# Kernel tuning notes

Hardware: AMD Instinct MI355X
Metric: run time of the kernel (lower is better)

The kernel has to match this reference:

```python
import jax, jax.numpy as jnp
import numpy as np
import math

IN_C, OUT_C, NUM_PARAM, STRIDE = 128, 256, 9, 1
BN_EPS = 1e-5


def _make_p_n(num_param):
    base_int = round(math.sqrt(num_param))
    row_number = num_param // base_int
    mod_number = num_param % base_int
    gx, gy = np.meshgrid(np.arange(row_number), np.arange(base_int), indexing='ij')
    px, py = gx.flatten(), gy.flatten()
    if mod_number > 0:
        mx, my = np.meshgrid(np.arange(row_number, row_number + 1), np.arange(mod_number), indexing='ij')
        px = np.concatenate([px, mx.flatten()])
        py = np.concatenate([py, my.flatten()])
    return np.concatenate([px, py]).astype(np.float32)  # (2N,)


def setup_inputs() -> dict:
    key = jax.random.key(0)
    ks = jax.random.split(key, 8)
    x = jax.random.normal(ks[0], (8, IN_C, 80, 80), dtype=jnp.float32)
    # offset-predicting conv (torch inits this to 0; use small random weights to exercise gathers)
    w_pconv = jax.random.normal(ks[1], (2 * NUM_PARAM, IN_C, 3, 3), dtype=jnp.float32) * 0.01
    b_pconv = jax.random.normal(ks[2], (2 * NUM_PARAM,), dtype=jnp.float32) * 0.1
    # final Conv: kernel (num_param, 1), stride (num_param, 1), pad 0, no bias
    w_conv = jax.random.normal(ks[3], (OUT_C, IN_C, NUM_PARAM, 1), dtype=jnp.float32) * (1.0 / math.sqrt(IN_C * NUM_PARAM))
    bn_gamma = jnp.ones((OUT_C,), jnp.float32) + 0.1 * jax.random.normal(ks[4], (OUT_C,), jnp.float32)
    bn_beta = 0.1 * jax.random.normal(ks[5], (OUT_C,), jnp.float32)
    bn_mean = 0.1 * jax.random.normal(ks[6], (OUT_C,), jnp.float32)
    bn_var = jnp.abs(jax.random.normal(ks[7], (OUT_C,), jnp.float32)) + 0.5
    p_n = jnp.asarray(_make_p_n(NUM_PARAM))
    return {"x": x, "w_pconv": w_pconv, "b_pconv": b_pconv, "w_conv": w_conv,
            "bn_gamma": bn_gamma, "bn_beta": bn_beta, "bn_mean": bn_mean,
            "bn_var": bn_var, "p_n": p_n}


def _conv2d(x, w, strides, padding):
    return jax.lax.conv_general_dilated(x, w, window_strides=strides, padding=padding,
                                        dimension_numbers=('NCHW', 'OIHW', 'NCHW'))


def reference(x, w_pconv, b_pconv, w_conv, bn_gamma, bn_beta, bn_mean, bn_var, p_n):
    b, c, H, W = x.shape
    # per-pixel offsets: [b, 2N, h, w]
    offset = _conv2d(x, w_pconv, (STRIDE, STRIDE), 'SAME') + b_pconv[None, :, None, None]
    N = offset.shape[1] // 2
    h, w = offset.shape[2], offset.shape[3]

    # sampling locations p = p_0 + p_n + offset
    px0 = jnp.broadcast_to((jnp.arange(h, dtype=x.dtype) * STRIDE)[None, None, :, None], (1, N, h, w))
    py0 = jnp.broadcast_to((jnp.arange(w, dtype=x.dtype) * STRIDE)[None, None, None, :], (1, N, h, w))
    p0 = jnp.concatenate([px0, py0], axis=1)  # [1, 2N, h, w]
    p = (p0 + p_n[None, :, None, None] + offset).transpose(0, 2, 3, 1)  # [b, h, w, 2N]

    def clamp2(t):
        return jnp.concatenate([jnp.clip(t[..., :N], 0, H - 1), jnp.clip(t[..., N:], 0, W - 1)], axis=-1)

    q_lt = clamp2(jnp.floor(p)).astype(jnp.int32)
    q_rb = clamp2(jnp.floor(p) + 1).astype(jnp.int32)
    q_lb = jnp.concatenate([q_lt[..., :N], q_rb[..., N:]], axis=-1)
    q_rt = jnp.concatenate([q_rb[..., :N], q_lt[..., N:]], axis=-1)
    pc = clamp2(p)

    # bilinear weights [b, h, w, N]
    def g(q, sx, sy):
        qf = q.astype(pc.dtype)
        return (1 + sx * (qf[..., :N] - pc[..., :N])) * (1 + sy * (qf[..., N:] - pc[..., N:]))

    g_lt, g_rb = g(q_lt, 1.0, 1.0), g(q_rb, -1.0, -1.0)
    g_lb, g_rt = g(q_lb, 1.0, -1.0), g(q_rt, -1.0, 1.0)

    x_flat = x.reshape(b, c, H * W)

    def gather(q):
        idx = (q[..., :N] * W + q[..., N:]).reshape(b, -1)  # [b, h*w*N]
        out = jax.vmap(lambda xf, i: xf[:, i])(x_flat, idx)  # [b, c, h*w*N]
        return out.reshape(b, c, h, w, N)

    x_off = (g_lt[:, None] * gather(q_lt) + g_rb[:, None] * gather(q_rb)
             + g_lb[:, None] * gather(q_lb) + g_rt[:, None] * gather(q_rt))

    # b c h w n -> b c (h n) w
    x_off = x_off.transpose(0, 1, 2, 4, 3).reshape(b, c, h * N, w)

    y = _conv2d(x_off, w_conv, (N, 1), 'VALID')  # [b, out_c, h, w]
    inv = jax.lax.rsqrt(bn_var + BN_EPS)
    y = (y - bn_mean[None, :, None, None]) * (bn_gamma * inv)[None, :, None, None] + bn_beta[None, :, None, None]
    return y * jax.nn.sigmoid(y)  # SiLU
```

## Files before the change

kernel.cpp:

```cpp
#include <hip/hip_runtime.h>
#include <hip/hip_bf16.h>


typedef __attribute__((ext_vector_type(8))) short bf16x8;
typedef __attribute__((ext_vector_type(4))) float f32x4;
typedef __attribute__((ext_vector_type(2))) float f32x2;
typedef __attribute__((ext_vector_type(4))) unsigned int u32x4;

#define NHW 6400
#define NPIX 80

__device__ __forceinline__ unsigned short f2bf(float f){
  __hip_bfloat16 h = __float2bfloat16(f);
  unsigned short u; __builtin_memcpy(&u, &h, 2); return u;
}
__device__ __forceinline__ f32x2 bfp2f(unsigned int u){
  union { unsigned int i; float f; } a, b;
  a.i = u << 16; b.i = u & 0xffff0000u;
  f32x2 r; r.x = a.f; r.y = b.f; return r;
}
__device__ __forceinline__ unsigned pk_bf16(float a, float b){
  unsigned r;
  asm("v_cvt_pk_bf16_f32 %0, %1, %2" : "=v"(r) : "v"(a), "v"(b));
  return r;
}
__device__ __forceinline__ void splitbf(float v, unsigned short& hi, unsigned short& lo){
  hi = f2bf(v);
  union { unsigned int i; float f; } h; h.i = (unsigned)hi << 16;
  lo = f2bf(v - h.f);
}
__device__ __forceinline__ float f16u2f(unsigned int u){
  unsigned short s = (unsigned short)u; _Float16 h;
  __builtin_memcpy(&h, &s, 2); return (float)h;
}
__device__ __forceinline__ unsigned short f2f16u(float f){
  _Float16 h = (_Float16)f; unsigned short s;
  __builtin_memcpy(&s, &h, 2); return s;
}
__device__ __forceinline__ float fast_silu(float v){
  float e, r;
  asm("v_exp_f32 %0, %1" : "=v"(e) : "v"(v * -1.44269504088896f));
  asm("v_rcp_f32 %0, %1" : "=v"(r) : "v"(1.0f + e));
  return v * r;
}

__global__ __launch_bounds__(256) void k_pre(const float* __restrict__ x,
                                             const float* __restrict__ w_conv,
                                             const float* __restrict__ w_pconv,
                                             const float* __restrict__ gamma,
                                             const float* __restrict__ beta,
                                             const float* __restrict__ mean,
                                             const float* __restrict__ var,
                                             unsigned short* __restrict__ xt,
                                             unsigned short* __restrict__ xtl,
                                             uint4* __restrict__ wf,
                                             uint4* __restrict__ wpfH,
                                             uint4* __restrict__ wpfL,
                                             float* __restrict__ shift){
  __shared__ unsigned short tileH[64 * 132];
  __shared__ unsigned short tileL[64 * 132];
  int blk = blockIdx.x; int t = threadIdx.x;
  if (blk < 800){
    int b = blk / 100; int pixbase = (blk % 100) * 64;
    int lane = t & 63; int cg = t >> 6;
    for (int ci = 0; ci < 32; ++ci){
      int c = cg * 32 + ci;
      float v = x[(b * 128 + c) * NHW + pixbase + lane];
      unsigned short hi, lo; splitbf(v, hi, lo);
      tileH[lane * 132 + c] = hi;
      tileL[lane * 132 + c] = lo;
    }
    __syncthreads();
    for (int i = 0; i < 8; ++i){
      int slot = t + i * 256; int m = slot >> 5; int c = (slot & 31) * 4;
      uint2 vH = *reinterpret_cast<const uint2*>(&tileH[m * 132 + c]);
      uint2 vL = *reinterpret_cast<const uint2*>(&tileL[m * 132 + c]);
      *reinterpret_cast<uint2*>(xt  + (b * NHW + pixbase + m) * 128 + c) = vH;
      *reinterpret_cast<uint2*>(xtl + (b * NHW + pixbase + m) * 128 + c) = vL;
    }
    return;
  }
  int pblk = blk - 800;
  if (pblk < 144){
    int id = pblk * 256 + t;
    int lane = id & 63, ofrag = (id >> 6) & 15, kc = (id >> 10) & 3, n = id >> 12;
    int o = ofrag * 16 + (lane & 15), cb = kc * 32 + ((lane >> 4) & 3) * 8;
    float sc = gamma[o] * rsqrtf(var[o] + 1e-5f);
    unsigned short h[8];
    for (int j = 0; j < 8; ++j) h[j] = f2bf(w_conv[(o * 128 + cb + j) * 9 + n] * sc);
    uint4 v;
    v.x = (unsigned)h[0] | ((unsigned)h[1] << 16);
    v.y = (unsigned)h[2] | ((unsigned)h[3] << 16);
    v.z = (unsigned)h[4] | ((unsigned)h[5] << 16);
    v.w = (unsigned)h[6] | ((unsigned)h[7] << 16);
    wf[id] = v;
  } else if (pblk < 180){
    int isLo = (pblk >= 162);
    int id = (pblk - (isLo ? 162 : 144)) * 256 + t;
    int lane = id & 63, ofrag = (id >> 6) & 1, kc = (id >> 7) & 3, tap = id >> 9;
    int o = ofrag * 16 + (lane & 15), cb = kc * 32 + ((lane >> 4) & 3) * 8;
    unsigned short h[8];
    for (int j = 0; j < 8; ++j){
      unsigned short hi = 0, lo = 0;
      if (o < 18) splitbf(w_pconv[(o * 128 + cb + j) * 9 + tap], hi, lo);
      h[j] = isLo ? lo : hi;
    }
    uint4 v;
    v.x = (unsigned)h[0] | ((unsigned)h[1] << 16);
    v.y = (unsigned)h[2] | ((unsigned)h[3] << 16);
    v.z = (unsigned)h[4] | ((unsigned)h[5] << 16);
    v.w = (unsigned)h[6] | ((unsigned)h[7] << 16);
    if (isLo) wpfL[id] = v; else wpfH[id] = v;
  } else {
    float sc = gamma[t] * rsqrtf(var[t] + 1e-5f);
    shift[t] = beta[t] - mean[t] * sc;
  }
}

__global__ __launch_bounds__(256, 4) void k_fused(const unsigned short* __restrict__ xt,
                                                  const unsigned short* __restrict__ xtl,
                                                  const uint4* __restrict__ wpfH,
                                                  const uint4* __restrict__ wpfL,
                                                  const float* __restrict__ bpc,
                                                  const float* __restrict__ pn,
                                                  const uint4* __restrict__ wf,
                                                  const float* __restrict__ shift,
                                                  float* __restrict__ out){
  int bid = blockIdx.x;
  int blk = (bid & 7) * 200 + (bid >> 3);
  int b = blk / 200; int pixbase = (blk % 200) * 32;
  int t = threadIdx.x; int lane = t & 63;

  __shared__ alignas(16) char smem[24576];
  short* BtileH  = (short*)(smem);
  short* BtileL  = (short*)(smem + 8704);
  float* off_lds = (float*)(smem + 17408);
  uint4* descL   = (uint4*)(smem + 19968);

  {
    int wv = t >> 6; int og = wv & 1; int pf = wv >> 1;
    f32x4 acc = (f32x4){0.f, 0.f, 0.f, 0.f};
    const unsigned short* xbH = xt  + (size_t)b * NHW * 128;
    const unsigned short* xbL = xtl + (size_t)b * NHW * 128;

    int m_i[4], c_i[4], h_i[4], w_i[4];
#pragma unroll
    for (int i = 0; i < 4; ++i){
      int slot = t + i * 256;
      m_i[i] = slot >> 5; c_i[i] = (slot & 31) * 4;
      int p = pixbase + m_i[i];
      h_i[i] = p / NPIX; w_i[i] = p % NPIX;
    }

    uint2 rH[4], rL[4];

#define LOADTAP(DH, DW)                                                        \
  _Pragma("unroll")                                                            \
  for (int i = 0; i < 4; ++i){                                                 \
    int h2 = h_i[i] + (DH), w2 = w_i[i] + (DW);                                \
    uint2 vH; vH.x = 0u; vH.y = 0u;                                            \
    uint2 vL; vL.x = 0u; vL.y = 0u;                                            \
    if ((unsigned)h2 < NPIX && (unsigned)w2 < NPIX){                           \
      int off = (h2 * NPIX + w2) * 128 + c_i[i];                               \
      vH = *reinterpret_cast<const uint2*>(xbH + off);                         \
      vL = *reinterpret_cast<const uint2*>(xbL + off);                         \
    }                                                                          \
    rH[i] = vH; rL[i] = vL;                                                    \
  }

#define WRITETILE()                                                            \
  _Pragma("unroll")                                                            \
  for (int i = 0; i < 4; ++i){                                                 \
    *reinterpret_cast<uint2*>(&BtileH[m_i[i] * 136 + c_i[i]]) = rH[i];         \
    *reinterpret_cast<uint2*>(&BtileL[m_i[i] * 136 + c_i[i]]) = rL[i];         \
  }

    LOADTAP(-1, -1)
    WRITETILE()
    __syncthreads();

#pragma unroll 1
    for (int tap = 0; tap < 9; ++tap){
      if (tap < 8){
        int dh2 = (tap + 1) / 3 - 1, dw2 = (tap + 1) % 3 - 1;
        LOADTAP(dh2, dw2)
      }
#pragma unroll
      for (int kc = 0; kc < 4; ++kc){
        int boff = (pf * 16 + (lane & 15)) * 136 + kc * 32 + ((lane >> 4) & 3) * 8;
        bf16x8 bH = *reinterpret_cast<const bf16x8*>(&BtileH[boff]);
        bf16x8 bL = *reinterpret_cast<const bf16x8*>(&BtileL[boff]);
        int widx = ((tap * 4 + kc) * 2 + og) * 64 + lane;
        bf16x8 aH = *reinterpret_cast<const bf16x8*>(&wpfH[widx]);
        bf16x8 aL = *reinterpret_cast<const bf16x8*>(&wpfL[widx]);
        acc = __builtin_amdgcn_mfma_f32_16x16x32_bf16(aH, bH, acc, 0, 0, 0);
        acc = __builtin_amdgcn_mfma_f32_16x16x32_bf16(aH, bL, acc, 0, 0, 0);
        acc = __builtin_amdgcn_mfma_f32_16x16x32_bf16(aL, bH, acc, 0, 0, 0);
        acc = __builtin_amdgcn_mfma_f32_16x16x32_bf16(aL, bL, acc, 0, 0, 0);
      }
      __syncthreads();
      if (tap < 8){
        WRITETILE()
        __syncthreads();
      }
    }

    int pl = pf * 16 + (lane & 15);
#pragma unroll
    for (int r = 0; r < 4; ++r){
      int o = og * 16 + ((lane >> 4) & 3) * 4 + r;
      if (o < 18) off_lds[pl * 20 + o] = acc[r] + bpc[o];
    }
    __syncthreads();

    for (int item = t; item < 288; item += 256){
      int m = item / 9, n = item % 9;
      int p = pixbase + m; int h = p / NPIX, w = p % NPIX;
      float px = (float)h + pn[n]     + off_lds[m * 20 + n];
      float py = (float)w + pn[9 + n] + off_lds[m * 20 + 9 + n];
      float flx = floorf(px), fly = floorf(py);
      float qltx = fminf(fmaxf(flx, 0.f), 79.f);
      float qrbx = fminf(fmaxf(flx + 1.f, 0.f), 79.f);
      float qlty = fminf(fmaxf(fly, 0.f), 79.f);
      float qrby = fminf(fmaxf(fly + 1.f, 0.f), 79.f);
      float pcx = fminf(fmaxf(px, 0.f), 79.f);
      float pcy = fminf(fmaxf(py, 0.f), 79.f);
      float dxl = 1.f + (qltx - pcx), dxr = 1.f - (qrbx - pcx);
      float dyl = 1.f + (qlty - pcy), dyr = 1.f - (qrby - pcy);
      unsigned ix_l = (unsigned)(int)qltx, ix_r = (unsigned)(int)qrbx;
      unsigned iy_l = (unsigned)(int)qlty, iy_r = (unsigned)(int)qrby;
      uint4 d;
      d.x = (ix_l * NPIX + iy_l) | ((ix_r * NPIX + iy_r) << 16);
      d.y = (ix_l * NPIX + iy_r) | ((ix_r * NPIX + iy_l) << 16);
      d.z = (unsigned)f2f16u(dxl * dyl) | ((unsigned)f2f16u(dxr * dyr) << 16);
      d.w = (unsigned)f2f16u(dxl * dyr) | ((unsigned)f2f16u(dxr * dyl) << 16);
      descL[n * 32 + m] = d;
    }
#undef LOADTAP
#undef WRITETILE
  }
  __syncthreads();
  __builtin_amdgcn_sched_barrier(0);

  {
    int ow = t >> 6;
    char* A_lds0 = smem;
    const char* xb = (const char*)(xt + (size_t)b * NHW * 128);

    int m0 = t >> 4;
    int m1 = m0 + 16;
    int cb = (t & 15) * 16;
    int ls0 = m0 * 256 + (cb ^ ((m0 & 7) << 4));
    int ls1 = m1 * 256 + (cb ^ ((m1 & 7) << 4));

    f32x4 acc[4][2];
#pragma unroll
    for (int of = 0; of < 4; ++of)
#pragma unroll
      for (int pf = 0; pf < 2; ++pf)
        acc[of][pf] = (f32x4){0.f, 0.f, 0.f, 0.f};

    u32x4 GX[4], GY[4];
    uint2 zwX, zwY;
    uint4 dB0, dB1;

#define DLD(N, M) descL[(N) * 32 + (M)]

#define ISSUE_X()                                                              \
  {                                                                            \
    zwX.x = dB0.z; zwX.y = dB0.w;                                              \
    GX[0] = *reinterpret_cast<const u32x4*>(xb + (dB0.x & 0xffffu) * 256u + (unsigned)cb); \
    GX[1] = *reinterpret_cast<const u32x4*>(xb + (dB0.x >> 16)     * 256u + (unsigned)cb); \
    GX[2] = *reinterpret_cast<const u32x4*>(xb + (dB0.y & 0xffffu) * 256u + (unsigned)cb); \
    GX[3] = *reinterpret_cast<const u32x4*>(xb + (dB0.y >> 16)     * 256u + (unsigned)cb); \
  }

#define ISSUE_Y()                                                              \
  {                                                                            \
    zwY.x = dB1.z; zwY.y = dB1.w;                                              \
    GY[0] = *reinterpret_cast<const u32x4*>(xb + (dB1.x & 0xffffu) * 256u + (unsigned)cb); \
    GY[1] = *reinterpret_cast<const u32x4*>(xb + (dB1.x >> 16)     * 256u + (unsigned)cb); \
    GY[2] = *reinterpret_cast<const u32x4*>(xb + (dB1.y & 0xffffu) * 256u + (unsigned)cb); \
    GY[3] = *reinterpret_cast<const u32x4*>(xb + (dB1.y >> 16)     * 256u + (unsigned)cb); \
  }

#define COMB(G, ZW, LSO, WB)                                                   \
  {                                                                            \
    float w0 = f16u2f(ZW.x & 0xffffu), w1 = f16u2f(ZW.x >> 16);                \
    float w2 = f16u2f(ZW.y & 0xffffu), w3 = f16u2f(ZW.y >> 16);                \
    u32x4 pk;                                                                  \
    _Pragma("unroll")                                                          \
    for (int j = 0; j < 4; ++j){                                               \
      f32x2 a = w0 * bfp2f(G[0][j]) + w1 * bfp2f(G[1][j])                      \
              + w2 * bfp2f(G[2][j]) + w3 * bfp2f(G[3][j]);                     \
      pk[j] = pk_bf16(a.x, a.y);                                               \
    }                                                                          \
    *reinterpret_cast<u32x4*>((WB) + (LSO)) = pk;                              \
  }

#define MFMA_HALF(NN, KCA, KCB)                                                \
  {                                                                            \
    const char* ab = A_lds0 + ((NN) & 1) * 8192;                               \
    __builtin_amdgcn_s_setprio(1);                                             \
    _Pragma("unroll")                                                          \
    for (int kc = (KCA); kc <= (KCB); ++kc){                                   \
      bf16x8 bfrk[2];                                                          \
      _Pragma("unroll")                                                        \
      for (int pf = 0; pf < 2; ++pf){                                          \
        int row = pf * 16 + (lane & 15);                                       \
        bfrk[pf] = *reinterpret_cast<const bf16x8*>(                           \
            ab + row * 256 + ((kc * 64 + ((lane >> 4) & 3) * 16) ^ ((row & 7) << 4))); \
      }                                                                        \
      _Pragma("unroll")                                                        \
      for (int of = 0; of < 4; ++of){                                          \
        bf16x8 afr = *reinterpret_cast<const bf16x8*>(                         \
            &wf[((((NN) * 4 + kc) * 16) + ow * 4 + of) * 64 + lane]);          \
        _Pragma("unroll")                                                      \
        for (int pf = 0; pf < 2; ++pf)                                         \
          acc[of][pf] = __builtin_amdgcn_mfma_f32_16x16x32_bf16(afr, bfrk[pf], acc[of][pf], 0, 0, 0); \
      }                                                                        \
    }                                                                          \
    __builtin_amdgcn_s_setprio(0);                                             \
  }

#define STEP(NN)                                                               \
  {                                                                            \
    if ((NN) < 8){ ISSUE_X() }                                                 \
    if ((NN) < 7){ dB0 = DLD((NN) + 2, m0); }                                  \
    MFMA_HALF(NN, 0, 1)                                                        \
    if ((NN) < 8){                                                             \
      COMB(GX, zwX, ls0, A_lds0 + (((NN) + 1) & 1) * 8192)                     \
      __builtin_amdgcn_sched_barrier(0);                                       \
      ISSUE_Y()                                                                \
    }                                                                          \
    if ((NN) < 7){ dB1 = DLD((NN) + 2, m1); }                                  \
    MFMA_HALF(NN, 2, 3)                                                        \
    if ((NN) < 8){                                                             \
      COMB(GY, zwY, ls1, A_lds0 + (((NN) + 1) & 1) * 8192)                     \
    }                                                                          \
    __syncthreads();                                                           \
  }

    dB0 = DLD(0, m0); dB1 = DLD(0, m1);
    ISSUE_X()
    COMB(GX, zwX, ls0, A_lds0)
    __builtin_amdgcn_sched_barrier(0);
    ISSUE_Y()
    COMB(GY, zwY, ls1, A_lds0)
    dB0 = DLD(1, m0); dB1 = DLD(1, m1);
    __syncthreads();

    STEP(0) STEP(1) STEP(2) STEP(3) STEP(4) STEP(5) STEP(6) STEP(7) STEP(8)

#pragma unroll
    for (int of = 0; of < 4; ++of)
#pragma unroll
      for (int pf = 0; pf < 2; ++pf){
        int pix = pixbase + pf * 16 + (lane & 15);
#pragma unroll
        for (int r = 0; r < 4; ++r){
          int o = ow * 64 + of * 16 + ((lane >> 4) & 3) * 4 + r;
          float v = acc[of][pf][r] + shift[o];
          out[(size_t)(b * 256 + o) * NHW + pix] = fast_silu(v);
        }
      }
#undef DLD
#undef ISSUE_X
#undef ISSUE_Y
#undef COMB
#undef MFMA_HALF
#undef STEP
  }
}

extern "C" void kernel_launch(void* const* d_in, const int* in_sizes, int n_in,
                              void* d_out, int out_size, void* d_ws, size_t ws_size,
                              hipStream_t stream){
  const float* x       = (const float*)d_in[0];
  const float* w_pconv = (const float*)d_in[1];
  const float* b_pconv = (const float*)d_in[2];
  const float* w_conv  = (const float*)d_in[3];
  const float* gamma   = (const float*)d_in[4];
  const float* beta    = (const float*)d_in[5];
  const float* mean    = (const float*)d_in[6];
  const float* var     = (const float*)d_in[7];
  const float* pn      = (const float*)d_in[8];

  char* ws = (char*)d_ws;
  unsigned short* xt  = (unsigned short*)(ws + 0);
  unsigned short* xtl = (unsigned short*)(ws + 13107200);
  uint4* wf           = (uint4*)(ws + 33587200);
  uint4* wpfH         = (uint4*)(ws + 34177024);
  uint4* wpfL         = (uint4*)(ws + 34250752);
  float* shift        = (float*)(ws + 34324480);
  float* out          = (float*)d_out;

  k_pre<<<981, 256, 0, stream>>>(x, w_conv, w_pconv, gamma, beta, mean, var,
                                 xt, xtl, wf, wpfH, wpfL, shift);
  k_fused<<<1600, 256, 0, stream>>>(xt, xtl, wpfH, wpfL, b_pconv, pn, wf, shift, out);
}
```

Measured before the change: 114.7 us.

## Gather bilinear samples directly into MFMA B fragments, dropping LDS staging and barriers

Second phase no longer stages the bilinearly combined samples in a double-buffered LDS tile. Each wave now gathers and combines its own B fragment in registers and feeds it straight to MFMA, so the per-tap __syncthreads and the LDS write/read round trip are gone. Waves are split into 2 pixel halves by 2 output halves (8 accumulators each, 128 outputs) instead of 4 output groups over 32 pixels. Work is redistributed as a result: each wave issues more gathers per MFMA, since pixel gathers are duplicated across the two output-half waves, and reuse of each gathered fragment is lower. LDS is also shrunk by overlapping off_lds with the tile region.

After: 211.7 us. +84.5%, slower.

```diff
diff --git a/kernel.cpp b/kernel.cpp
--- a/kernel.cpp
+++ b/kernel.cpp
@@ -131,11 +131,11 @@
   int b = blk / 200; int pixbase = (blk % 200) * 32;
   int t = threadIdx.x; int lane = t & 63;
 
-  __shared__ alignas(16) char smem[24576];
+  __shared__ alignas(16) char smem[22016];
   short* BtileH  = (short*)(smem);
   short* BtileL  = (short*)(smem + 8704);
-  float* off_lds = (float*)(smem + 17408);
-  uint4* descL   = (uint4*)(smem + 19968);
+  float* off_lds = (float*)(smem);
+  uint4* descL   = (uint4*)(smem + 17408);
 
   {
     int wv = t >> 6; int og = wv & 1; int pf = wv >> 1;
@@ -243,132 +243,97 @@
   __builtin_amdgcn_sched_barrier(0);
 
   {
-    int ow = t >> 6;
-    char* A_lds0 = smem;
+    int wv = t >> 6;
+    int pxh = wv & 1;
+    int oh  = wv >> 1;
+    int pxl = lane & 15;
+    unsigned coff = (unsigned)((lane >> 4) * 16);
+    int didx = pxh * 16 + pxl;
     const char* xb = (const char*)(xt + (size_t)b * NHW * 128);
 
-    int m0 = t >> 4;
-    int m1 = m0 + 16;
-    int cb = (t & 15) * 16;
-    int ls0 = m0 * 256 + (cb ^ ((m0 & 7) << 4));
-    int ls1 = m1 * 256 + (cb ^ ((m1 & 7) << 4));
-
-    f32x4 acc[4][2];
-#pragma unroll
-    for (int of = 0; of < 4; ++of)
-#pragma unroll
-      for (int pf = 0; pf < 2; ++pf)
-        acc[of][pf] = (f32x4){0.f, 0.f, 0.f, 0.f};
-
-    u32x4 GX[4], GY[4];
-    uint2 zwX, zwY;
-    uint4 dB0, dB1;
-
-#define DLD(N, M) descL[(N) * 32 + (M)]
-
-#define ISSUE_X()                                                              \
+    f32x4 acc[8];
+#pragma unroll
+    for (int of = 0; of < 8; ++of) acc[of] = (f32x4){0.f, 0.f, 0.f, 0.f};
+
+    u32x4 Ga[4], Gb[4];
+    uint4 dcur, dnxt;
+    float cw0, cw1, cw2, cw3, nw0, nw1, nw2, nw3;
+    bf16x8 Bf;
+
+#define GATHER(G, D, KC)                                                       \
   {                                                                            \
-    zwX.x = dB0.z; zwX.y = dB0.w;                                              \
-    GX[0] = *reinterpret_cast<const u32x4*>(xb + (dB0.x & 0xffffu) * 256u + (unsigned)cb); \
-    GX[1] = *reinterpret_cast<const u32x4*>(xb + (dB0.x >> 16)     * 256u + (unsigned)cb); \
-    GX[2] = *reinterpret_cast<const u32x4*>(xb + (dB0.y & 0xffffu) * 256u + (unsigned)cb); \
-    GX[3] = *reinterpret_cast<const u32x4*>(xb + (dB0.y >> 16)     * 256u + (unsigned)cb); \
-  }
-
-#define ISSUE_Y()                                                              \
+    G[0] = *reinterpret_cast<const u32x4*>(xb + (D.x & 0xffffu) * 256u + (KC) * 64u + coff); \
+    G[1] = *reinterpret_cast<const u32x4*>(xb + (D.x >> 16)     * 256u + (KC) * 64u + coff); \
+    G[2] = *reinterpret_cast<const u32x4*>(xb + (D.y & 0xffffu) * 256u + (KC) * 64u + coff); \
+    G[3] = *reinterpret_cast<const u32x4*>(xb + (D.y >> 16)     * 256u + (KC) * 64u + coff); \
+  }
+
+#define COMBINE(G)                                                             \
   {                                                                            \
-    zwY.x = dB1.z; zwY.y = dB1.w;                                              \
-    GY[0] = *reinterpret_cast<const u32x4*>(xb + (dB1.x & 0xffffu) * 256u + (unsigned)cb); \
-    GY[1] = *reinterpret_cast<const u32x4*>(xb + (dB1.x >> 16)     * 256u + (unsigned)cb); \
-    GY[2] = *reinterpret_cast<const u32x4*>(xb + (dB1.y & 0xffffu) * 256u + (unsigned)cb); \
-    GY[3] = *reinterpret_cast<const u32x4*>(xb + (dB1.y >> 16)     * 256u + (unsigned)cb); \
-  }
-
-#define COMB(G, ZW, LSO, WB)                                                   \
-  {                                                                            \
-    float w0 = f16u2f(ZW.x & 0xffffu), w1 = f16u2f(ZW.x >> 16);                \
-    float w2 = f16u2f(ZW.y & 0xffffu), w3 = f16u2f(ZW.y >> 16);                \
     u32x4 pk;                                                                  \
     _Pragma("unroll")                                                          \
     for (int j = 0; j < 4; ++j){                                               \
-      f32x2 a = w0 * bfp2f(G[0][j]) + w1 * bfp2f(G[1][j])                      \
-              + w2 * bfp2f(G[2][j]) + w3 * bfp2f(G[3][j]);                     \
+      f32x2 a = cw0 * bfp2f(G[0][j]) + cw1 * bfp2f(G[1][j])                    \
+              + cw2 * bfp2f(G[2][j]) + cw3 * bfp2f(G[3][j]);                   \
       pk[j] = pk_bf16(a.x, a.y);                                               \
     }                                                                          \
-    *reinterpret_cast<u32x4*>((WB) + (LSO)) = pk;                              \
-  }
-
-#define MFMA_HALF(NN, KCA, KCB)                                                \
+    Bf = __builtin_bit_cast(bf16x8, pk);                                       \
+  }
+
+#define MFMA8(NN, KC)                                                          \
   {                                                                            \
-    const char* ab = A_lds0 + ((NN) & 1) * 8192;                               \
     __builtin_amdgcn_s_setprio(1);                                             \
     _Pragma("unroll")                                                          \
-    for (int kc = (KCA); kc <= (KCB); ++kc){                                   \
-      bf16x8 bfrk[2];                                                          \
-      _Pragma("unroll")                                                        \
-      for (int pf = 0; pf < 2; ++pf){                                          \
-        int row = pf * 16 + (lane & 15);                                       \
-        bfrk[pf] = *reinterpret_cast<const bf16x8*>(                           \
-            ab + row * 256 + ((kc * 64 + ((lane >> 4) & 3) * 16) ^ ((row & 7) << 4))); \
-      }                                                                        \
-      _Pragma("unroll")                                                        \
-      for (int of = 0; of < 4; ++of){                                          \
-        bf16x8 afr = *reinterpret_cast<const bf16x8*>(                         \
-            &wf[((((NN) * 4 + kc) * 16) + ow * 4 + of) * 64 + lane]);          \
-        _Pragma("unroll")                                                      \
-        for (int pf = 0; pf < 2; ++pf)                                         \
-          acc[of][pf] = __builtin_amdgcn_mfma_f32_16x16x32_bf16(afr, bfrk[pf], acc[of][pf], 0, 0, 0); \
-      }                                                                        \
+    for (int of = 0; of < 8; ++of){                                            \
+      bf16x8 afr = *reinterpret_cast<const bf16x8*>(                           \
+          &wf[(((NN) * 4 + (KC)) * 16 + oh * 8 + of) * 64 + lane]);            \
+      acc[of] = __builtin_amdgcn_mfma_f32_16x16x32_bf16(afr, Bf, acc[of], 0, 0, 0); \
     }                                                                          \
     __builtin_amdgcn_s_setprio(0);                                             \
   }
 
 #define STEP(NN)                                                               \
   {                                                                            \
-    if ((NN) < 8){ ISSUE_X() }                                                 \
-    if ((NN) < 7){ dB0 = DLD((NN) + 2, m0); }                                  \
-    MFMA_HALF(NN, 0, 1)                                                        \
+    GATHER(Gb, dcur, 1)                                                        \
+    __builtin_amdgcn_sched_barrier(0);                                         \
+    COMBINE(Ga) MFMA8(NN, 0)                                                   \
+    GATHER(Ga, dcur, 2)                                                        \
+    if ((NN) < 8){ dnxt = descL[((NN) + 1) * 32 + didx]; }                     \
+    __builtin_amdgcn_sched_barrier(0);                                         \
+    COMBINE(Gb) MFMA8(NN, 1)                                                   \
+    GATHER(Gb, dcur, 3)                                                        \
+    __builtin_amdgcn_sched_barrier(0);                                         \
+    COMBINE(Ga) MFMA8(NN, 2)                                                   \
     if ((NN) < 8){                                                             \
-      COMB(GX, zwX, ls0, A_lds0 + (((NN) + 1) & 1) * 8192)                     \
-      __builtin_amdgcn_sched_barrier(0);                                       \
-      ISSUE_Y()                                                                \
+      nw0 = f16u2f(dnxt.z & 0xffffu); nw1 = f16u2f(dnxt.z >> 16);              \
+      nw2 = f16u2f(dnxt.w & 0xffffu); nw3 = f16u2f(dnxt.w >> 16);              \
+      GATHER(Ga, dnxt, 0)                                                      \
     }                                                                          \
-    if ((NN) < 7){ dB1 = DLD((NN) + 2, m1); }                                  \
-    MFMA_HALF(NN, 2, 3)                                                        \
-    if ((NN) < 8){                                                             \
-      COMB(GY, zwY, ls1, A_lds0 + (((NN) + 1) & 1) * 8192)                     \
-    }                                                                          \
-    __syncthreads();                                                           \
-  }
-
-    dB0 = DLD(0, m0); dB1 = DLD(0, m1);
-    ISSUE_X()
-    COMB(GX, zwX, ls0, A_lds0)
-    __builtin_amdgcn_sched_barrier(0);
-    ISSUE_Y()
-    COMB(GY, zwY, ls1, A_lds0)
-    dB0 = DLD(1, m0); dB1 = DLD(1, m1);
-    __syncthreads();
+    __builtin_amdgcn_sched_barrier(0);                                         \
+    COMBINE(Gb) MFMA8(NN, 3)                                                   \
+    if ((NN) < 8){ dcur = dnxt; cw0 = nw0; cw1 = nw1; cw2 = nw2; cw3 = nw3; }  \
+  }
+
+    dcur = descL[didx];
+    cw0 = f16u2f(dcur.z & 0xffffu); cw1 = f16u2f(dcur.z >> 16);
+    cw2 = f16u2f(dcur.w & 0xffffu); cw3 = f16u2f(dcur.w >> 16);
+    GATHER(Ga, dcur, 0)
 
     STEP(0) STEP(1) STEP(2) STEP(3) STEP(4) STEP(5) STEP(6) STEP(7) STEP(8)
 
 #pragma unroll
-    for (int of = 0; of < 4; ++of)
-#pragma unroll
-      for (int pf = 0; pf < 2; ++pf){
-        int pix = pixbase + pf * 16 + (lane & 15);
-#pragma unroll
-        for (int r = 0; r < 4; ++r){
-          int o = ow * 64 + of * 16 + ((lane >> 4) & 3) * 4 + r;
-          float v = acc[of][pf][r] + shift[o];
-          out[(size_t)(b * 256 + o) * NHW + pix] = fast_silu(v);
-        }
+    for (int of = 0; of < 8; ++of){
+      int o = oh * 128 + of * 16 + (lane >> 4) * 4;
+      int pix = pixbase + pxh * 16 + pxl;
+#pragma unroll
+      for (int r = 0; r < 4; ++r){
+        float v = acc[of][r] + shift[o + r];
+        out[(size_t)(b * 256 + o + r) * NHW + pix] = fast_silu(v);
       }
-#undef DLD
-#undef ISSUE_X
-#undef ISSUE_Y
-#undef COMB
-#undef MFMA_HALF
+    }
+#undef GATHER
+#undef COMBINE
+#undef MFMA8
 #undef STEP
   }
 }
```

## Prefetch gathers a full step ahead and preload next tap's weight fragments

Applied to the files above, without the earlier changes.

Reworks the software pipeline of the deformable-conv GEMM loop. The X and Y bilinear gathers for step N+2 are now issued at the end of step N, a whole MFMA step before they are combined, and the descriptors move one step further ahead. The first half of the next tap's weight fragments is also preloaded into registers so the MFMAs do not wait on global weight loads. The aim is to hide gather and weight latency behind the matrix work, at the cost of more live registers, which may reduce occupancy or cause spills.

Result: no change. 116.0 us (+1.2%).

```diff
diff --git a/kernel.cpp b/kernel.cpp
--- a/kernel.cpp
+++ b/kernel.cpp
@@ -263,6 +263,7 @@
     u32x4 GX[4], GY[4];
     uint2 zwX, zwY;
     uint4 dB0, dB1;
+    bf16x8 W01[8];
 
 #define DLD(N, M) descL[(N) * 32 + (M)]
 
@@ -298,12 +299,46 @@
     *reinterpret_cast<u32x4*>((WB) + (LSO)) = pk;                              \
   }
 
-#define MFMA_HALF(NN, KCA, KCB)                                                \
+#define WLOAD01(NN)                                                            \
+  {                                                                            \
+    _Pragma("unroll")                                                          \
+    for (int j = 0; j < 8; ++j){                                               \
+      int kc = j >> 2; int of = j & 3;                                         \
+      W01[j] = *reinterpret_cast<const bf16x8*>(                               \
+          &wf[((((NN) * 4 + kc) * 16) + ow * 4 + of) * 64 + lane]);            \
+    }                                                                          \
+  }
+
+#define MFMA_P01(NN)                                                           \
   {                                                                            \
     const char* ab = A_lds0 + ((NN) & 1) * 8192;                               \
     __builtin_amdgcn_s_setprio(1);                                             \
     _Pragma("unroll")                                                          \
-    for (int kc = (KCA); kc <= (KCB); ++kc){                                   \
+    for (int kc = 0; kc <= 1; ++kc){                                           \
+      bf16x8 bfrk[2];                                                          \
+      _Pragma("unroll")                                                        \
+      for (int pf = 0; pf < 2; ++pf){                                          \
+        int row = pf * 16 + (lane & 15);                                       \
+        bfrk[pf] = *reinterpret_cast<const bf16x8*>(                           \
+            ab + row * 256 + ((kc * 64 + ((lane >> 4) & 3) * 16) ^ ((row & 7) << 4))); \
+      }                                                                        \
+      _Pragma("unroll")                                                        \
+      for (int of = 0; of < 4; ++of){                                          \
+        bf16x8 afr = W01[kc * 4 + of];                                         \
+        _Pragma("unroll")                                                      \
+        for (int pf = 0; pf < 2; ++pf)                                         \
+          acc[of][pf] = __builtin_amdgcn_mfma_f32_16x16x32_bf16(afr, bfrk[pf], acc[of][pf], 0, 0, 0); \
+      }                                                                        \
+    }                                                                          \
+    __builtin_amdgcn_s_setprio(0);                                             \
+  }
+
+#define MFMA_S23(NN)                                                           \
+  {                                                                            \
+    const char* ab = A_lds0 + ((NN) & 1) * 8192;                               \
+    __builtin_amdgcn_s_setprio(1);                                             \
+    _Pragma("unroll")                                                          \
+    for (int kc = 2; kc <= 3; ++kc){                                           \
       bf16x8 bfrk[2];                                                          \
       _Pragma("unroll")                                                        \
       for (int pf = 0; pf < 2; ++pf){                                          \
@@ -325,29 +360,31 @@
 
 #define STEP(NN)                                                               \
   {                                                                            \
-    if ((NN) < 8){ ISSUE_X() }                                                 \
-    if ((NN) < 7){ dB0 = DLD((NN) + 2, m0); }                                  \
-    MFMA_HALF(NN, 0, 1)                                                        \
+    MFMA_P01(NN)                                                               \
     if ((NN) < 8){                                                             \
       COMB(GX, zwX, ls0, A_lds0 + (((NN) + 1) & 1) * 8192)                     \
-      __builtin_amdgcn_sched_barrier(0);                                       \
-      ISSUE_Y()                                                                \
-    }                                                                          \
-    if ((NN) < 7){ dB1 = DLD((NN) + 2, m1); }                                  \
-    MFMA_HALF(NN, 2, 3)                                                        \
-    if ((NN) < 8){                                                             \
       COMB(GY, zwY, ls1, A_lds0 + (((NN) + 1) & 1) * 8192)                     \
     }                                                                          \
+    __builtin_amdgcn_sched_barrier(0);                                         \
+    if ((NN) < 8){ WLOAD01((NN) + 1) }                                         \
+    __builtin_amdgcn_sched_barrier(0);                                         \
+    MFMA_S23(NN)                                                               \
+    __builtin_amdgcn_sched_barrier(0);                                         \
+    if ((NN) < 7){ ISSUE_X() ISSUE_Y() }                                       \
+    if ((NN) < 6){ dB0 = DLD((NN) + 3, m0); dB1 = DLD((NN) + 3, m1); }         \
     __syncthreads();                                                           \
   }
 
     dB0 = DLD(0, m0); dB1 = DLD(0, m1);
-    ISSUE_X()
+    ISSUE_X() ISSUE_Y()
     COMB(GX, zwX, ls0, A_lds0)
-    __builtin_amdgcn_sched_barrier(0);
-    ISSUE_Y()
     COMB(GY, zwY, ls1, A_lds0)
     dB0 = DLD(1, m0); dB1 = DLD(1, m1);
+    __builtin_amdgcn_sched_barrier(0);
+    WLOAD01(0)
+    __builtin_amdgcn_sched_barrier(0);
+    ISSUE_X() ISSUE_Y()
+    dB0 = DLD(2, m0); dB1 = DLD(2, m1);
     __syncthreads();
 
     STEP(0) STEP(1) STEP(2) STEP(3) STEP(4) STEP(5) STEP(6) STEP(7) STEP(8)
@@ -368,7 +405,9 @@
 #undef ISSUE_X
 #undef ISSUE_Y
 #undef COMB
-#undef MFMA_HALF
+#undef WLOAD01
+#undef MFMA_P01
+#undef MFMA_S23
 #undef STEP
   }
 }
```

## Split fused deformable conv into offset-conv, gather, and GEMM kernels

Applied to the files above, without the earlier changes.

Replaces the single fused kernel with three kernels. The first computes offsets and writes packed bilinear descriptors, the second gathers and interpolates the sampled features into a bf16 buffer, and the third runs the MFMA GEMM with the BN+SiLU epilogue. This is meant to remove the occupancy and serialization limits of doing offset conv, gather and GEMM in one block. In exchange it writes and re-reads about 118 MB of intermediate x_off through global memory, and it falls back to the fused path when the workspace is too small.

Result: slower. 186.5 us (+62.6%).

```diff
diff --git a/kernel.cpp b/kernel.cpp
--- a/kernel.cpp
+++ b/kernel.cpp
@@ -117,6 +117,229 @@
   }
 }
 
+__global__ __launch_bounds__(256, 6) void k_offconv(const unsigned short* __restrict__ xt,
+                                                    const unsigned short* __restrict__ xtl,
+                                                    const uint4* __restrict__ wpfH,
+                                                    const uint4* __restrict__ wpfL,
+                                                    const float* __restrict__ bpc,
+                                                    const float* __restrict__ pn,
+                                                    uint4* __restrict__ desc){
+  int bid = blockIdx.x;
+  int blk = (bid & 7) * 200 + (bid >> 3);
+  int b = blk / 200; int pixbase = (blk % 200) * 32;
+  int t = threadIdx.x; int lane = t & 63; int wv = t >> 6;
+  int og = wv & 1;
+  int pf = wv >> 1;
+  __shared__ short BtileH[32 * 136];
+  __shared__ short BtileL[32 * 136];
+  __shared__ float off_lds[32 * 20];
+
+  f32x4 acc = (f32x4){0.f, 0.f, 0.f, 0.f};
+  const unsigned short* xbH = xt  + (size_t)b * NHW * 128;
+  const unsigned short* xbL = xtl + (size_t)b * NHW * 128;
+
+  int m_i[4], c_i[4], h_i[4], w_i[4];
+#pragma unroll
+  for (int i = 0; i < 4; ++i){
+    int slot = t + i * 256;
+    m_i[i] = slot >> 5; c_i[i] = (slot & 31) * 4;
+    int p = pixbase + m_i[i];
+    h_i[i] = p / NPIX; w_i[i] = p % NPIX;
+  }
+
+  uint2 rH[4], rL[4];
+
+#define LOADTAP(DH, DW)                                                        \
+  _Pragma("unroll")                                                            \
+  for (int i = 0; i < 4; ++i){                                                 \
+    int h2 = h_i[i] + (DH), w2 = w_i[i] + (DW);                                \
+    uint2 vH; vH.x = 0u; vH.y = 0u;                                            \
+    uint2 vL; vL.x = 0u; vL.y = 0u;                                            \
+    if ((unsigned)h2 < NPIX && (unsigned)w2 < NPIX){                           \
+      int off = (h2 * NPIX + w2) * 128 + c_i[i];                               \
+      vH = *reinterpret_cast<const uint2*>(xbH + off);                         \
+      vL = *reinterpret_cast<const uint2*>(xbL + off);                         \
+    }                                                                          \
+    rH[i] = vH; rL[i] = vL;                                                    \
+  }
+
+#define WRITETILE()                                                            \
+  _Pragma("unroll")                                                            \
+  for (int i = 0; i < 4; ++i){                                                 \
+    *reinterpret_cast<uint2*>(&BtileH[m_i[i] * 136 + c_i[i]]) = rH[i];         \
+    *reinterpret_cast<uint2*>(&BtileL[m_i[i] * 136 + c_i[i]]) = rL[i];         \
+  }
+
+  LOADTAP(-1, -1)
+  WRITETILE()
+  __syncthreads();
+
+#pragma unroll 1
+  for (int tap = 0; tap < 9; ++tap){
+    if (tap < 8){
+      int dh2 = (tap + 1) / 3 - 1, dw2 = (tap + 1) % 3 - 1;
+      LOADTAP(dh2, dw2)
+    }
+#pragma unroll
+    for (int kc = 0; kc < 4; ++kc){
+      int boff = (pf * 16 + (lane & 15)) * 136 + kc * 32 + ((lane >> 4) & 3) * 8;
+      bf16x8 bH = *reinterpret_cast<const bf16x8*>(&BtileH[boff]);
+      bf16x8 bL = *reinterpret_cast<const bf16x8*>(&BtileL[boff]);
+      int widx = ((tap * 4 + kc) * 2 + og) * 64 + lane;
+      bf16x8 aH = *reinterpret_cast<const bf16x8*>(&wpfH[widx]);
+      bf16x8 aL = *reinterpret_cast<const bf16x8*>(&wpfL[widx]);
+      acc = __builtin_amdgcn_mfma_f32_16x16x32_bf16(aH, bH, acc, 0, 0, 0);
+      acc = __builtin_amdgcn_mfma_f32_16x16x32_bf16(aH, bL, acc, 0, 0, 0);
+      acc = __builtin_amdgcn_mfma_f32_16x16x32_bf16(aL, bH, acc, 0, 0, 0);
+      acc = __builtin_amdgcn_mfma_f32_16x16x32_bf16(aL, bL, acc, 0, 0, 0);
+    }
+    __syncthreads();
+    if (tap < 8){
+      WRITETILE()
+      __syncthreads();
+    }
+  }
+
+  int pl = pf * 16 + (lane & 15);
+#pragma unroll
+  for (int r = 0; r < 4; ++r){
+    int o = og * 16 + ((lane >> 4) & 3) * 4 + r;
+    if (o < 18) off_lds[pl * 20 + o] = acc[r] + bpc[o];
+  }
+  __syncthreads();
+
+  for (int item = t; item < 288; item += 256){
+    int m = item / 9, n = item % 9;
+    int p = pixbase + m; int h = p / NPIX, w = p % NPIX;
+    float px = (float)h + pn[n]     + off_lds[m * 20 + n];
+    float py = (float)w + pn[9 + n] + off_lds[m * 20 + 9 + n];
+    float flx = floorf(px), fly = floorf(py);
+    float qltx = fminf(fmaxf(flx, 0.f), 79.f);
+    float qrbx = fminf(fmaxf(flx + 1.f, 0.f), 79.f);
+    float qlty = fminf(fmaxf(fly, 0.f), 79.f);
+    float qrby = fminf(fmaxf(fly + 1.f, 0.f), 79.f);
+    float pcx = fminf(fmaxf(px, 0.f), 79.f);
+    float pcy = fminf(fmaxf(py, 0.f), 79.f);
+    float dxl = 1.f + (qltx - pcx), dxr = 1.f - (qrbx - pcx);
+    float dyl = 1.f + (qlty - pcy), dyr = 1.f - (qrby - pcy);
+    unsigned ix_l = (unsigned)(int)qltx, ix_r = (unsigned)(int)qrbx;
+    unsigned iy_l = (unsigned)(int)qlty, iy_r = (unsigned)(int)qrby;
+    uint4 d;
+    d.x = (ix_l * NPIX + iy_l) | ((ix_r * NPIX + iy_r) << 16);
+    d.y = (ix_l * NPIX + iy_r) | ((ix_r * NPIX + iy_l) << 16);
+    d.z = (unsigned)f2f16u(dxl * dyl) | ((unsigned)f2f16u(dxr * dyr) << 16);
+    d.w = (unsigned)f2f16u(dxl * dyr) | ((unsigned)f2f16u(dxr * dyl) << 16);
+    desc[(size_t)(b * 9 + n) * NHW + p] = d;
+  }
+#undef LOADTAP
+#undef WRITETILE
+}
+
+__global__ __launch_bounds__(256) void k_gather(const unsigned short* __restrict__ xt,
+                                                const uint4* __restrict__ desc,
+                                                char* __restrict__ x_off){
+  int bid = blockIdx.x; int t = threadIdx.x; int lane = t & 63; int wv = t >> 6;
+  __shared__ alignas(16) char tr[4][4352];
+  int u = bid * 4 + wv;
+  int b = u / 3600; int rem = u % 3600; int n = rem / 400; int pxt = rem % 400;
+  const uint4* db = desc + (size_t)(b * 9 + n) * NHW + pxt * 16;
+  const char* xb = (const char*)(xt + (size_t)b * NHW * 128);
+  char* xo = x_off + ((size_t)((b * 9 + n) * 400 + pxt)) * 4096;
+  int g = lane >> 4;
+  unsigned cbv = (unsigned)((lane & 15) * 16);
+  char* wb = &tr[wv][0];
+
+#define GATH(G, D)                                                             \
+  {                                                                            \
+    G[0] = *reinterpret_cast<const u32x4*>(xb + (D.x & 0xffffu) * 256u + cbv); \
+    G[1] = *reinterpret_cast<const u32x4*>(xb + (D.x >> 16)     * 256u + cbv); \
+    G[2] = *reinterpret_cast<const u32x4*>(xb + (D.y & 0xffffu) * 256u + cbv); \
+    G[3] = *reinterpret_cast<const u32x4*>(xb + (D.y >> 16)     * 256u + cbv); \
+  }
+
+#define COMBW(G, D, S)                                                         \
+  {                                                                            \
+    float w0 = f16u2f(D.z & 0xffffu), w1 = f16u2f(D.z >> 16);                  \
+    float w2 = f16u2f(D.w & 0xffffu), w3 = f16u2f(D.w >> 16);                  \
+    u32x4 pk;                                                                  \
+    _Pragma("unroll")                                                          \
+    for (int j = 0; j < 4; ++j){                                               \
+      f32x2 a = w0 * bfp2f(G[0][j]) + w1 * bfp2f(G[1][j])                      \
+              + w2 * bfp2f(G[2][j]) + w3 * bfp2f(G[3][j]);                     \
+      pk[j] = pk_bf16(a.x, a.y);                                               \
+    }                                                                          \
+    *reinterpret_cast<u32x4*>(wb + ((S) * 4 + g) * 272 + cbv) = pk;            \
+  }
+
+  uint4 d0 = db[g], d1 = db[4 + g], d2 = db[8 + g], d3 = db[12 + g];
+  u32x4 Ga[4], Gb[4];
+  GATH(Ga, d0) GATH(Gb, d1)
+  COMBW(Ga, d0, 0) GATH(Ga, d2)
+  COMBW(Gb, d1, 1) GATH(Gb, d3)
+  COMBW(Ga, d2, 2)
+  COMBW(Gb, d3, 3)
+
+#pragma unroll
+  for (int kc = 0; kc < 4; ++kc){
+    u32x4 v = *reinterpret_cast<const u32x4*>(wb + (lane & 15) * 272 + kc * 64 + g * 16);
+    *reinterpret_cast<u32x4*>(xo + kc * 1024 + lane * 16) = v;
+  }
+#undef GATH
+#undef COMBW
+}
+
+__global__ __launch_bounds__(256, 4) void k_gemm(const char* __restrict__ x_off,
+                                                 const uint4* __restrict__ wf,
+                                                 const float* __restrict__ shift,
+                                                 float* __restrict__ out){
+  int bid = blockIdx.x; int t = threadIdx.x; int lane = t & 63; int wv = t >> 6;
+  int u = bid * 4 + wv;
+  int b = u / 400; int pxt = u % 400;
+  const char* xob = x_off + ((size_t)b * 9 * 400 + pxt) * 4096;
+
+  f32x4 acc[16];
+#pragma unroll
+  for (int of = 0; of < 16; ++of) acc[of] = (f32x4){0.f, 0.f, 0.f, 0.f};
+
+  bf16x8 Bc, Bn;
+  Bc = *reinterpret_cast<const bf16x8*>(xob + lane * 16);
+
+#pragma unroll 4
+  for (int c = 0; c < 36; ++c){
+    if (c < 35){
+      int c1 = c + 1; int n1 = c1 >> 2, kc1 = c1 & 3;
+      Bn = *reinterpret_cast<const bf16x8*>(xob + (size_t)n1 * 1638400 + kc1 * 1024 + lane * 16);
+    }
+    __builtin_amdgcn_s_setprio(1);
+#pragma unroll
+    for (int og = 0; og < 4; ++og){
+      bf16x8 a0 = *reinterpret_cast<const bf16x8*>(&wf[(c * 16 + og * 4 + 0) * 64 + lane]);
+      bf16x8 a1 = *reinterpret_cast<const bf16x8*>(&wf[(c * 16 + og * 4 + 1) * 64 + lane]);
+      bf16x8 a2 = *reinterpret_cast<const bf16x8*>(&wf[(c * 16 + og * 4 + 2) * 64 + lane]);
+      bf16x8 a3 = *reinterpret_cast<const bf16x8*>(&wf[(c * 16 + og * 4 + 3) * 64 + lane]);
+      acc[og * 4 + 0] = __builtin_amdgcn_mfma_f32_16x16x32_bf16(a0, Bc, acc[og * 4 + 0], 0, 0, 0);
+      acc[og * 4 + 1] = __builtin_amdgcn_mfma_f32_16x16x32_bf16(a1, Bc, acc[og * 4 + 1], 0, 0, 0);
+      acc[og * 4 + 2] = __builtin_amdgcn_mfma_f32_16x16x32_bf16(a2, Bc, acc[og * 4 + 2], 0, 0, 0);
+      acc[og * 4 + 3] = __builtin_amdgcn_mfma_f32_16x16x32_bf16(a3, Bc, acc[og * 4 + 3], 0, 0, 0);
+      __builtin_amdgcn_sched_barrier(0);
+    }
+    __builtin_amdgcn_s_setprio(0);
+    Bc = Bn;
+  }
+
+  int px = pxt * 16 + (lane & 15);
+#pragma unroll
+  for (int of = 0; of < 16; ++of){
+    int oc0 = of * 16 + (lane >> 4) * 4;
+#pragma unroll
+    for (int r = 0; r < 4; ++r){
+      int oc = oc0 + r;
+      float v = acc[of][r] + shift[oc];
+      out[((size_t)b * 256 + oc) * NHW + px] = fast_silu(v);
+    }
+  }
+}
+
 __global__ __launch_bounds__(256, 4) void k_fused(const unsigned short* __restrict__ xt,
                                                   const unsigned short* __restrict__ xtl,
                                                   const uint4* __restrict__ wpfH,
@@ -389,13 +612,23 @@
   char* ws = (char*)d_ws;
   unsigned short* xt  = (unsigned short*)(ws + 0);
   unsigned short* xtl = (unsigned short*)(ws + 13107200);
+  uint4* desc         = (uint4*)(ws + 26214400);
   uint4* wf           = (uint4*)(ws + 33587200);
   uint4* wpfH         = (uint4*)(ws + 34177024);
   uint4* wpfL         = (uint4*)(ws + 34250752);
   float* shift        = (float*)(ws + 34324480);
+  char*  x_off        = (char*)(ws + 34325504);
   float* out          = (float*)d_out;
+
+  const size_t NEED = 34325504ull + 117964800ull;
 
   k_pre<<<981, 256, 0, stream>>>(x, w_conv, w_pconv, gamma, beta, mean, var,
                                  xt, xtl, wf, wpfH, wpfL, shift);
-  k_fused<<<1600, 256, 0, stream>>>(xt, xtl, wpfH, wpfL, b_pconv, pn, wf, shift, out);
-}
+  if (ws_size >= NEED){
+    k_offconv<<<1600, 256, 0, stream>>>(xt, xtl, wpfH, wpfL, b_pconv, pn, desc);
+    k_gather<<<7200, 256, 0, stream>>>(xt, desc, x_off);
+    k_gemm<<<800, 256, 0, stream>>>(x_off, wf, shift, out);
+  } else {
+    k_fused<<<1600, 256, 0, stream>>>(xt, xtl, wpfH, wpfL, b_pconv, pn, wf, shift, out);
+  }
+}
```
